# Performance work log

Measured on AMD Instinct MI355X. Metric: run time of the kernel, lower is better.

The kernel has to match this reference:

```python
import jax, jax.numpy as jnp
import numpy as np
import math

# Dimensions (match init_kwargs config)
N = 32768          # num_nodes
E = N * 16         # num_edges
D = 256            # hidden_dim == bigru output_dim (input_proj is DxD)
H = 8              # num_heads
DH = 32            # head_dim
TD = H * DH        # total_dim
FFN = 1024         # ffn_dim
L = 2              # num_layers
EPS = 1e-5


def setup_inputs() -> dict:
    key = jax.random.key(0)
    ks = jax.random.split(key, 16)
    w = lambda k, *s: jax.random.normal(k, s, dtype=jnp.float32) * 0.02
    return {
        "x": jax.random.normal(ks[0], (N, D), dtype=jnp.float32),
        "edge_index": jax.random.randint(ks[1], (2, E), 0, N, dtype=jnp.int64).astype(jnp.int32),
        "w_in": w(ks[2], D, D), "b_in": jnp.zeros((D,), jnp.float32),
        "ln1_g": jnp.ones((L, D), jnp.float32), "ln1_b": jnp.zeros((L, D), jnp.float32),
        "ln2_g": jnp.ones((L, D), jnp.float32), "ln2_b": jnp.zeros((L, D), jnp.float32),
        "wq": w(ks[3], L, D, TD), "bq": jnp.zeros((L, TD), jnp.float32),
        "wk": w(ks[4], L, D, TD), "bk": jnp.zeros((L, TD), jnp.float32),
        "wv": w(ks[5], L, D, TD), "bv": jnp.zeros((L, TD), jnp.float32),
        "wo": w(ks[6], L, TD, D), "bo": jnp.zeros((L, D), jnp.float32),
        "w1": w(ks[7], L, D, FFN), "b1": jnp.zeros((L, FFN), jnp.float32),
        "w2": w(ks[8], L, FFN, D), "b2": jnp.zeros((L, D), jnp.float32),
    }


def _layernorm(x, g, b):
    mu = jnp.mean(x, axis=-1, keepdims=True)
    var = jnp.mean(jnp.square(x - mu), axis=-1, keepdims=True)
    return (x - mu) * jax.lax.rsqrt(var + EPS) * g + b


def reference(x, edge_index, w_in, b_in, ln1_g, ln1_b, ln2_g, ln2_b,
              wq, bq, wk, bk, wv, bv, wo, bo, w1, b1, w2, b2):
    n = x.shape[0]
    src0, dst0 = edge_index[0], edge_index[1]
    # in-degree (nodes with no in-edges output zeros from attention, per torch loop)
    deg = jax.ops.segment_sum(jnp.ones_like(src0, jnp.float32), dst0, num_segments=n)
    # append self edge per node (torch appends `node` to its own neighbor list)
    ar = jnp.arange(n, dtype=src0.dtype)
    src = jnp.concatenate([src0, ar])
    dst = jnp.concatenate([dst0, ar])

    h = x @ w_in + b_in  # input_proj
    scale = 1.0 / math.sqrt(DH)
    for l in range(L):
        xn = _layernorm(h, ln1_g[l], ln1_b[l])
        q = (xn @ wq[l] + bq[l]).reshape(n, H, DH)
        k = (xn @ wk[l] + bk[l]).reshape(n, H, DH)
        v = (xn @ wv[l] + bv[l]).reshape(n, H, DH)
        # edge-parallel scaled-dot attention with segment softmax over dst
        scores = jnp.einsum('ehd,ehd->eh', q[dst], k[src]) * scale  # [E+N, H]
        m = jax.ops.segment_max(scores, dst, num_segments=n)        # [N, H]
        ex = jnp.exp(scores - m[dst])
        z = jax.ops.segment_sum(ex, dst, num_segments=n)            # [N, H]
        attn = ex / z[dst]
        agg = jax.ops.segment_sum(attn[:, :, None] * v[src], dst, num_segments=n)  # [N, H, DH]
        agg = jnp.where((deg > 0)[:, None, None], agg, 0.0)
        h = h + agg.reshape(n, TD) @ wo[l] + bo[l] * jnp.where(deg > 0, 1.0, 1.0)[:, None] * 0 + (agg.reshape(n, TD) @ wo[l] * 0)  # placeholder removed below
        # note: o_proj bias always applied in torch (o_proj of masked agg)
        h = h - (agg.reshape(n, TD) @ wo[l])  # undo accidental double-add above
        h = h + (agg.reshape(n, TD) @ wo[l] + bo[l]) - bo[l] * 0
        xn2 = _layernorm(h, ln2_g[l], ln2_b[l])
        ffn = jax.nn.gelu(xn2 @ w1[l] + b1[l], approximate=False) @ w2[l] + b2[l]
        h = h + ffn
    return h
```

## Files before the change

### kernel.cpp

```cpp
#include <hip/hip_runtime.h>
#include <hip/hip_bf16.h>
#include <math.h>

typedef __bf16 bf16_t;
typedef __bf16 bf16x4 __attribute__((ext_vector_type(4)));
typedef __bf16 bf16x8 __attribute__((ext_vector_type(8)));
typedef float f32x4 __attribute__((ext_vector_type(4)));
typedef float f32x2 __attribute__((ext_vector_type(2)));

static constexpr int N_NODES = 32768;
static constexpr int N_EDGES = N_NODES * 16;

#define GLB_PTR(p) ((const __attribute__((address_space(1))) void*)(p))
#define LDS_PTR(p) ((__attribute__((address_space(3))) void*)(p))

__device__ __forceinline__ float load_ext(const void* p, long i, int fl) {
  if (fl == 2) return 0.f;
  return fl ? (float)((const bf16_t*)p)[i] : ((const float*)p)[i];
}

struct SniffArgs {
  const void* ptr[20];
  int elems[20];
  int kind[20];
};

__global__ __launch_bounds__(256) void sniff_all(SniffArgs a, int* flags) {
  int b = blockIdx.x;
  int t = threadIdx.x;
  __shared__ int s1[256], s2[256];
  if (a.kind[b] == 0) {
    const unsigned short* p = (const unsigned short*)a.ptr[b];
    int pairs = min(1024, a.elems[b] / 2);
    int sane = 0, nz = 0;
    for (int i = t; i < pairs; i += 256) {
      unsigned short we = p[2 * i], wo = p[2 * i + 1];
      if (we | wo) nz++;
      int e = (we >> 7) & 0xFF;
      if (we != 0 && e >= 100 && e <= 140) sane++;
    }
    s1[t] = sane; s2[t] = nz;
    __syncthreads();
    for (int o = 128; o >= 1; o >>= 1) {
      if (t < o) { s1[t] += s1[t + o]; s2[t] += s2[t + o]; }
      __syncthreads();
    }
    if (t == 0)
      flags[b] = (s2[0] == 0) ? 2 : ((2 * s1[0] > pairs) ? 1 : 0);
  } else {
    const int* ip = (const int*)a.ptr[b];
    int n = min(512, a.elems[b] / 2);
    int zeros = 0;
    for (int i = t; i < n; i += 256)
      if (ip[2 * i + 1] == 0) zeros++;
    s1[t] = zeros;
    __syncthreads();
    for (int o = 128; o >= 1; o >>= 1) {
      if (t < o) s1[t] += s1[t + o];
      __syncthreads();
    }
    if (t == 0) flags[b] = (s1[0] * 4 > n * 3) ? 1 : 0;
  }
}

__global__ __launch_bounds__(256) void convert_x(const void* src, bf16_t* dst,
                                                 const int* flagp) {
  int fl = *flagp;
  int i = (blockIdx.x * 256 + threadIdx.x) * 4;
  if (fl == 1) {
    *(int2*)(dst + i) = *(const int2*)((const bf16_t*)src + i);
  } else if (fl == 0) {
    float4 v = *(const float4*)((const float*)src + i);
    dst[i] = (bf16_t)v.x; dst[i + 1] = (bf16_t)v.y;
    dst[i + 2] = (bf16_t)v.z; dst[i + 3] = (bf16_t)v.w;
  } else {
    dst[i] = (bf16_t)0.f; dst[i + 1] = (bf16_t)0.f;
    dst[i + 2] = (bf16_t)0.f; dst[i + 3] = (bf16_t)0.f;
  }
}

struct TransDesc { const void* src; long soff; bf16_t* dst; int K; int N; int tile0; int fidx; };
struct TransArgs { TransDesc d[13]; const int* flags; };

__global__ __launch_bounds__(256) void transpose_many(TransArgs args) {
  __shared__ bf16_t tile[32][33];
  int blk = blockIdx.x;
  int i = 0;
#pragma unroll
  for (int j = 1; j < 13; ++j)
    if (blk >= args.d[j].tile0) i = j;
  TransDesc dd = args.d[i];
  int fl = args.flags[dd.fidx];
  int t = blk - dd.tile0;
  int tiles_x = dd.N / 32;
  int nbase = (t % tiles_x) * 32;
  int kbase = (t / tiles_x) * 32;
  int tx = threadIdx.x & 31, ty = threadIdx.x >> 5;
#pragma unroll
  for (int j = 0; j < 32; j += 8)
    tile[ty + j][tx] = (bf16_t)load_ext(dd.src, dd.soff + (long)(kbase + ty + j) * dd.N + nbase + tx, fl);
  __syncthreads();
#pragma unroll
  for (int j = 0; j < 32; j += 8)
    dd.dst[(size_t)(nbase + ty + j) * dd.K + kbase + tx] = tile[tx][ty + j];
}

__device__ __forceinline__ int edge_at(const void* ei, long i, int fl64) {
  return fl64 ? (int)((const long long*)ei)[i] : ((const int*)ei)[i];
}

__global__ __launch_bounds__(256) void deg_count(const void* __restrict__ ei,
                                                 const int* flagp,
                                                 int* __restrict__ deg) {
  int fl = *flagp;
  int e = blockIdx.x * 256 + threadIdx.x;
  if (e < N_EDGES) atomicAdd(&deg[edge_at(ei, (long)N_EDGES + e, fl)], 1);
}

__global__ __launch_bounds__(1024) void scan_offsets(const int* __restrict__ deg,
                                                     int* __restrict__ off) {
  __shared__ int s[1024];
  int t = threadIdx.x;
  int base = t * 32;
  int sum = 0;
  for (int i = 0; i < 32; ++i) sum += deg[base + i];
  s[t] = sum;
  __syncthreads();
  for (int o = 1; o < 1024; o <<= 1) {
    int v = (t >= o) ? s[t - o] : 0;
    __syncthreads();
    s[t] += v;
    __syncthreads();
  }
  int run = s[t] - sum;
  for (int i = 0; i < 32; ++i) { off[base + i] = run; run += deg[base + i]; }
  if (t == 1023) off[N_NODES] = run;
}

__global__ __launch_bounds__(256) void scatter_edges(const void* __restrict__ ei,
                                                     const int* flagp,
                                                     const int* __restrict__ off,
                                                     int* __restrict__ cursor,
                                                     int* __restrict__ csr) {
  int fl = *flagp;
  int e = blockIdx.x * 256 + threadIdx.x;
  if (e < N_EDGES) {
    int d = edge_at(ei, (long)N_EDGES + e, fl);
    int p = off[d] + atomicAdd(&cursor[d], 1);
    csr[p] = edge_at(ei, e, fl);
  }
}

__device__ __forceinline__ int attn_slot(int j, int ne, int nid, int sl,
                                         const int* __restrict__ csr, int e0) {
  return (j == ne - 1) ? nid : (j < 32 ? __shfl(sl, j, 32) : csr[e0 + j]);
}

__device__ __forceinline__ void attn_load4(const unsigned char* __restrict__ qkv8,
                                           int c0, int ne, int nid, int sl,
                                           const int* __restrict__ csr, int e0, int l32,
                                           uint2 (&bk)[4], uint2 (&bv)[4]) {
#pragma unroll
  for (int t = 0; t < 4; ++t) {
    int j = c0 + t;
    if (j < ne) {
      int s = attn_slot(j, ne, nid, sl, csr, e0);
      const unsigned char* row = qkv8 + ((size_t)(s * 3) << 8) + l32 * 8;
      bk[t] = *(const uint2*)(row + 256);
      bv[t] = *(const uint2*)(row + 512);
    }
  }
}

__device__ __forceinline__ void attn_proc4(int c0, int ne,
                                           const f32x2& q01, const f32x2& q23,
                                           const f32x2& q45, const f32x2& q67,
                                           const uint2 (&bk)[4], const uint2 (&bv)[4],
                                           f32x2& a01, f32x2& a23, f32x2& a45, f32x2& a67,
                                           float& l) {
  const float C = 0.25503398f;
#pragma unroll
  for (int t = 0; t < 4; ++t) {
    int j = c0 + t;
    if (j < ne) {
      uint2 kr = bk[t], vr = bv[t];
      f32x2 d = q01 * __builtin_amdgcn_cvt_pk_f32_fp8(kr.x, 0);
      d += q23 * __builtin_amdgcn_cvt_pk_f32_fp8(kr.x, 1);
      d += q45 * __builtin_amdgcn_cvt_pk_f32_fp8(kr.y, 0);
      d += q67 * __builtin_amdgcn_cvt_pk_f32_fp8(kr.y, 1);
      float p = d[0] + d[1];
      p += __shfl_xor(p, 1);
      p += __shfl_xor(p, 2);
      float ev = __builtin_amdgcn_exp2f(fminf(p * C, 86.f));
      f32x2 ev2 = {ev, ev};
      a01 += ev2 * __builtin_amdgcn_cvt_pk_f32_fp8(vr.x, 0);
      a23 += ev2 * __builtin_amdgcn_cvt_pk_f32_fp8(vr.x, 1);
      a45 += ev2 * __builtin_amdgcn_cvt_pk_f32_fp8(vr.y, 0);
      a67 += ev2 * __builtin_amdgcn_cvt_pk_f32_fp8(vr.y, 1);
      l += ev;
    }
  }
}

__global__ __launch_bounds__(256) void attn_k(const unsigned char* __restrict__ qkv8,
                                              const int* __restrict__ off,
                                              const int* __restrict__ csr,
                                              const int* __restrict__ deg,
                                              bf16_t* __restrict__ agg) {
  const int sub = threadIdx.x >> 5;
  const int nid = blockIdx.x * 8 + sub;
  const int l32 = threadIdx.x & 31;

  const unsigned char* nb = qkv8 + (size_t)((nid * 3) << 8);
  uint2 qw = *(const uint2*)(nb + l32 * 8);
  f32x2 q01 = __builtin_amdgcn_cvt_pk_f32_fp8(qw.x, 0);
  f32x2 q23 = __builtin_amdgcn_cvt_pk_f32_fp8(qw.x, 1);
  f32x2 q45 = __builtin_amdgcn_cvt_pk_f32_fp8(qw.y, 0);
  f32x2 q67 = __builtin_amdgcn_cvt_pk_f32_fp8(qw.y, 1);

  const int e0 = off[nid], e1 = off[nid + 1];
  const int ne = e1 - e0 + 1;
  int sl = (l32 < ne - 1) ? csr[e0 + l32] : nid;

  uint2 kA[4], vA[4], kB[4], vB[4];
  float l = 0.f;
  f32x2 a01 = {0.f, 0.f}, a23 = {0.f, 0.f}, a45 = {0.f, 0.f}, a67 = {0.f, 0.f};

  attn_load4(qkv8, 0, ne, nid, sl, csr, e0, l32, kA, vA);
  for (int c = 0; c < ne; c += 8) {
    attn_load4(qkv8, c + 4, ne, nid, sl, csr, e0, l32, kB, vB);
    attn_proc4(c, ne, q01, q23, q45, q67, kA, vA, a01, a23, a45, a67, l);
    attn_load4(qkv8, c + 8, ne, nid, sl, csr, e0, l32, kA, vA);
    attn_proc4(c + 4, ne, q01, q23, q45, q67, kB, vB, a01, a23, a45, a67, l);
  }

  float inv = (deg[nid] > 0) ? 1.f / l : 0.f;
  bf16x8 ov;
  ov[0] = (bf16_t)(a01[0] * inv); ov[1] = (bf16_t)(a01[1] * inv);
  ov[2] = (bf16_t)(a23[0] * inv); ov[3] = (bf16_t)(a23[1] * inv);
  ov[4] = (bf16_t)(a45[0] * inv); ov[5] = (bf16_t)(a45[1] * inv);
  ov[6] = (bf16_t)(a67[0] * inv); ov[7] = (bf16_t)(a67[1] * inv);
  *(bf16x8*)(agg + (size_t)nid * 256 + l32 * 8) = ov;
}

template <int MODE, bool FUSED3>
__global__ __launch_bounds__(256) void gemm_kernel(const bf16_t* __restrict__ A,
                                                   const bf16_t* __restrict__ BT,
                                                   const void* b0, const void* b1, const void* b2,
                                                   long boff,
                                                   const int* f0, const int* f1, const int* f2,
                                                   void* __restrict__ Cout,
                                                   float* __restrict__ out2,
                                                   int N, int K) {
  const int fl0 = *f0;
  const int fl1 = FUSED3 ? *f1 : 0;
  const int fl2 = FUSED3 ? *f2 : 0;
  const int bm = blockIdx.y * 128;
  const int bn = blockIdx.x * 128;
  const int tid = threadIdx.x;
  const int lane = tid & 63;
  const int wid = tid >> 6;
  const int wr = wid >> 1, wc = wid & 1;
  const int lrow = lane & 15;
  const int lquad = lane >> 4;
  const int l8 = lane >> 3;
  const int u = lane & 7;

  __shared__ __align__(16) bf16_t As[128 * 64];
  __shared__ __align__(16) bf16_t Bs[128 * 64];

  const bf16_t* aptr[4];
  const bf16_t* bptr[4];
#pragma unroll
  for (int c = 0; c < 4; ++c) {
    int row = (wid * 4 + c) * 8 + l8;
    int kseg = (u ^ l8) << 3;
    aptr[c] = A + (size_t)(bm + row) * K + kseg;
    bptr[c] = BT + (size_t)(bn + row) * K + kseg;
  }

  f32x4 acc[4][4];
#pragma unroll
  for (int i = 0; i < 4; i++)
#pragma unroll
    for (int j = 0; j < 4; j++)
#pragma unroll
      for (int r = 0; r < 4; r++) acc[i][j][r] = 0.f;

  for (int k0 = 0; k0 < K; k0 += 64) {
#pragma unroll
    for (int c = 0; c < 4; ++c) {
      int chunk = wid * 4 + c;
      __builtin_amdgcn_global_load_lds(GLB_PTR(aptr[c] + k0), LDS_PTR(As + chunk * 512), 16, 0, 0);
      __builtin_amdgcn_global_load_lds(GLB_PTR(bptr[c] + k0), LDS_PTR(Bs + chunk * 512), 16, 0, 0);
    }
    __syncthreads();
#pragma unroll
    for (int ks = 0; ks < 2; ++ks) {
      bf16x8 a[4], b[4];
#pragma unroll
      for (int i = 0; i < 4; i++) {
        int pu = ((ks * 4 + lquad) ^ (lrow & 7)) * 8;
        a[i] = *(const bf16x8*)(&As[(wr * 64 + i * 16 + lrow) * 64 + pu]);
        b[i] = *(const bf16x8*)(&Bs[(wc * 64 + i * 16 + lrow) * 64 + pu]);
      }
#pragma unroll
      for (int i = 0; i < 4; i++)
#pragma unroll
        for (int j = 0; j < 4; j++)
          acc[i][j] = __builtin_amdgcn_mfma_f32_16x16x32_bf16(a[i], b[j], acc[i][j], 0, 0, 0);
    }
    __syncthreads();
  }

#pragma unroll
  for (int j = 0; j < 4; j++) {
    int n = bn + wc * 64 + j * 16 + lrow;
    float bv;
    if (FUSED3) {
      int seg = n >> 8;
      const void* bp = (seg == 0) ? b0 : ((seg == 1) ? b1 : b2);
      int fl = (seg == 0) ? fl0 : ((seg == 1) ? fl1 : fl2);
      bv = load_ext(bp, boff + (n & 255), fl);
    } else {
      bv = load_ext(b0, boff + n, fl0);
    }
#pragma unroll
    for (int i = 0; i < 4; i++) {
      int m0 = bm + wr * 64 + i * 16 + lquad * 4;
#pragma unroll
      for (int r = 0; r < 4; r++) {
        float val = acc[i][j][r] + bv;
        size_t idx = (size_t)(m0 + r) * N + n;
        if (MODE == 0) {
          ((bf16_t*)Cout)[idx] = (bf16_t)val;
        } else if (MODE == 1) {
          float gl = 0.5f * val * (1.f + erff(val * 0.7071067811865475f));
          ((bf16_t*)Cout)[idx] = (bf16_t)gl;
        } else if (MODE == 4) {
          out2[idx] = ((const float*)Cout)[idx] + val;
        } else if (MODE == 7) {
          unsigned pk = __builtin_amdgcn_cvt_pk_fp8_f32(val, val, 0u, false);
          ((unsigned char*)Cout)[idx] = (unsigned char)(pk & 0xFF);
        }
      }
    }
  }
}

template <bool RES>
__global__ __launch_bounds__(256) void gemm_ln(const bf16_t* __restrict__ A,
                                               const bf16_t* __restrict__ BT,
                                               const void* bias, long boff, const int* bfp,
                                               const void* g, long goff, const int* gfp,
                                               const void* bv2, long bvoff, const int* bvfp,
                                               float* __restrict__ h,
                                               bf16_t* __restrict__ xn,
                                               int K) {
  const int flb = *bfp, flg = *gfp, flbv = *bvfp;
  const int bm = blockIdx.y * 32;
  const int tid = threadIdx.x;
  const int lane = tid & 63;
  const int wid = tid >> 6;
  const int lrow = lane & 15;
  const int lquad = lane >> 4;
  const int l8 = lane >> 3;
  const int u = lane & 7;

  __shared__ __align__(16) bf16_t As[32 * 64];
  __shared__ __align__(16) bf16_t Bs[256 * 64];
  __shared__ float sums[32][4], sqs[32][4];
  __shared__ float mus[32], rss[32];

  const bf16_t* aptr = A + (size_t)(bm + wid * 8 + l8) * K + ((u ^ l8) << 3);
  const bf16_t* bptr[8];
#pragma unroll
  for (int c = 0; c < 8; ++c) {
    int chunk = wid * 8 + c;
    bptr[c] = BT + (size_t)(chunk * 8 + l8) * K + ((u ^ l8) << 3);
  }

  f32x4 acc[2][4];
#pragma unroll
  for (int i = 0; i < 2; i++)
#pragma unroll
    for (int j = 0; j < 4; j++)
#pragma unroll
      for (int r = 0; r < 4; r++) acc[i][j][r] = 0.f;

  for (int k0 = 0; k0 < K; k0 += 64) {
    __builtin_amdgcn_global_load_lds(GLB_PTR(aptr + k0), LDS_PTR(As + wid * 512), 16, 0, 0);
#pragma unroll
    for (int c = 0; c < 8; ++c)
      __builtin_amdgcn_global_load_lds(GLB_PTR(bptr[c] + k0), LDS_PTR(Bs + (wid * 8 + c) * 512), 16, 0, 0);
    __syncthreads();
#pragma unroll
    for (int ks = 0; ks < 2; ++ks) {
      bf16x8 a[2], b[4];
      int pu = ((ks * 4 + lquad) ^ (lrow & 7)) * 8;
#pragma unroll
      for (int i = 0; i < 2; i++)
        a[i] = *(const bf16x8*)(&As[(i * 16 + lrow) * 64 + pu]);
#pragma unroll
      for (int j = 0; j < 4; j++)
        b[j] = *(const bf16x8*)(&Bs[(wid * 64 + j * 16 + lrow) * 64 + pu]);
#pragma unroll
      for (int i = 0; i < 2; i++)
#pragma unroll
        for (int j = 0; j < 4; j++)
          acc[i][j] = __builtin_amdgcn_mfma_f32_16x16x32_bf16(a[i], b[j], acc[i][j], 0, 0, 0);
    }
    __syncthreads();
  }

#pragma unroll
  for (int j = 0; j < 4; j++) {
    int n = wid * 64 + j * 16 + lrow;
    float bvv = load_ext(bias, boff + n, flb);
#pragma unroll
    for (int i = 0; i < 2; i++) {
      int rl = i * 16 + lquad * 4;
#pragma unroll
      for (int r = 0; r < 4; r++) {
        float v = acc[i][j][r] + bvv;
        size_t idx = (size_t)(bm + rl + r) * 256 + n;
        if (RES) v += h[idx];
        acc[i][j][r] = v;
        h[idx] = v;
      }
    }
  }
#pragma unroll
  for (int i = 0; i < 2; i++) {
#pragma unroll
    for (int r = 0; r < 4; r++) {
      float s = acc[i][0][r] + acc[i][1][r] + acc[i][2][r] + acc[i][3][r];
      float q = acc[i][0][r] * acc[i][0][r] + acc[i][1][r] * acc[i][1][r]
              + acc[i][2][r] * acc[i][2][r] + acc[i][3][r] * acc[i][3][r];
#pragma unroll
      for (int o = 1; o <= 8; o <<= 1) {
        s += __shfl_xor(s, o);
        q += __shfl_xor(q, o);
      }
      if (lrow == 0) {
        int row = i * 16 + lquad * 4 + r;
        sums[row][wid] = s;
        sqs[row][wid] = q;
      }
    }
  }
  __syncthreads();
  if (tid < 32) {
    float s = sums[tid][0] + sums[tid][1] + sums[tid][2] + sums[tid][3];
    float q = sqs[tid][0] + sqs[tid][1] + sqs[tid][2] + sqs[tid][3];
    float mu = s * (1.f / 256.f);
    float var = q * (1.f / 256.f) - mu * mu;
    mus[tid] = mu;
    rss[tid] = rsqrtf(var + 1e-5f);
  }
  __syncthreads();
#pragma unroll
  for (int j = 0; j < 4; j++) {
    int n = wid * 64 + j * 16 + lrow;
    float gv = load_ext(g, goff + n, flg);
    float bb = load_ext(bv2, bvoff + n, flbv);
#pragma unroll
    for (int i = 0; i < 2; i++) {
#pragma unroll
      for (int r = 0; r < 4; r++) {
        int row = i * 16 + lquad * 4 + r;
        float xv = (acc[i][j][r] - mus[row]) * rss[row] * gv + bb;
        xn[(size_t)(bm + row) * 256 + n] = (bf16_t)xv;
      }
    }
  }
}

extern "C" void kernel_launch(void* const* d_in, const int* in_sizes, int n_in,
                              void* d_out, int out_size, void* d_ws, size_t ws_size,
                              hipStream_t stream) {
  const void* ei = d_in[1];

  char* ws = (char*)d_ws;
  size_t o = 0;
  int* flags  = (int*)(ws + o);    o += 256;
  int* deg    = (int*)(ws + o);    o += (size_t)N_NODES * 4;
  int* cursor = (int*)(ws + o);    o += (size_t)N_NODES * 4;
  int* off    = (int*)(ws + o);    o += 131328;
  int* csr    = (int*)(ws + o);    o += (size_t)N_EDGES * 4;
  bf16_t* wT  = (bf16_t*)(ws + o); o += (size_t)1638400 * 2;
  float* h    = (float*)(ws + o);  o += (size_t)N_NODES * 256 * 4;
  bf16_t* xn  = (bf16_t*)(ws + o); o += (size_t)N_NODES * 256 * 2;
  bf16_t* big = (bf16_t*)(ws + o); o += (size_t)N_NODES * 1024 * 2;
  bf16_t* xb = big;
  unsigned char* qkv8 = (unsigned char*)big;
  bf16_t* ab = xn;
  bf16_t* ffnb = big;

  hipMemsetAsync(deg, 0, N_NODES * 4, stream);
  hipMemsetAsync(cursor, 0, N_NODES * 4, stream);

  SniffArgs sa;
  for (int b = 0; b < 20; ++b) {
    sa.ptr[b] = d_in[b];
    sa.elems[b] = in_sizes[b];
    sa.kind[b] = (b == 1) ? 1 : 0;
  }
  sniff_all<<<20, 256, 0, stream>>>(sa, flags);

  convert_x<<<(N_NODES * 256) / 1024, 256, 0, stream>>>(d_in[0], xb, flags + 0);

  TransArgs ta;
  ta.flags = flags;
  int tiles = 0, idx = 0;
  auto add = [&](int slot, long soff, bf16_t* dst, int K, int N) {
    ta.d[idx].src = d_in[slot]; ta.d[idx].soff = soff; ta.d[idx].dst = dst;
    ta.d[idx].K = K; ta.d[idx].N = N; ta.d[idx].tile0 = tiles; ta.d[idx].fidx = slot;
    tiles += (K / 32) * (N / 32);
    ++idx;
  };
  bf16_t* wTin = wT;
  auto layer_base = [&](int l) { return wT + 65536 + (size_t)l * 786432; };
  add(2, 0, wTin, 256, 256);
  for (int l = 0; l < 2; ++l) {
    bf16_t* base = layer_base(l);
    add(8,  (long)l * 65536,  base + 0,      256, 256);
    add(10, (long)l * 65536,  base + 65536,  256, 256);
    add(12, (long)l * 65536,  base + 131072, 256, 256);
    add(14, (long)l * 65536,  base + 196608, 256, 256);
    add(16, (long)l * 262144, base + 262144, 256, 1024);
    add(18, (long)l * 262144, base + 524288, 1024, 256);
  }
  transpose_many<<<tiles, 256, 0, stream>>>(ta);

  deg_count<<<N_EDGES / 256, 256, 0, stream>>>(ei, flags + 1, deg);
  scan_offsets<<<1, 1024, 0, stream>>>(deg, off);
  scatter_edges<<<N_EDGES / 256, 256, 0, stream>>>(ei, flags + 1, off, cursor, csr);

  gemm_ln<false><<<dim3(1, 1024), 256, 0, stream>>>(
      xb, wTin, d_in[3], 0, flags + 3,
      d_in[4], 0, flags + 4, d_in[5], 0, flags + 5, h, xn, 256);

  for (int l = 0; l < 2; ++l) {
    bf16_t* base = layer_base(l);
    gemm_kernel<7, true><<<dim3(6, 256), 256, 0, stream>>>(
        xn, base, d_in[9], d_in[11], d_in[13], (long)l * 256,
        flags + 9, flags + 11, flags + 13, qkv8, nullptr, 768, 256);
    attn_k<<<N_NODES / 8, 256, 0, stream>>>(qkv8, off, csr, deg, ab);
    gemm_ln<true><<<dim3(1, 1024), 256, 0, stream>>>(
        ab, base + 196608, d_in[15], (long)l * 256, flags + 15,
        d_in[6], (long)l * 256, flags + 6, d_in[7], (long)l * 256, flags + 7,
        h, xn, 256);
    gemm_kernel<1, false><<<dim3(8, 256), 256, 0, stream>>>(
        xn, base + 262144, d_in[17], nullptr, nullptr, (long)l * 1024,
        flags + 17, flags + 17, flags + 17, ffnb, nullptr, 1024, 256);
    if (l == 0) {
      gemm_ln<true><<<dim3(1, 1024), 256, 0, stream>>>(
          ffnb, base + 524288, d_in[19], 0, flags + 19,
          d_in[4], 256, flags + 4, d_in[5], 256, flags + 5, h, xn, 1024);
    } else {
      gemm_kernel<4, false><<<dim3(2, 256), 256, 0, stream>>>(
          ffnb, base + 524288, d_in[19], nullptr, nullptr, (long)l * 256,
          flags + 19, flags + 19, flags + 19, h, (float*)d_out, 256, 1024);
    }
  }
}
```

Baseline: 633.7 us.

## Stage GEMM epilogue through LDS for coalesced stores and remap blocks per XCD

The GEMM epilogue for the bf16/GELU/fp8 modes now writes the output tile into shared memory first. It then copies it to global memory as 16-byte row-contiguous stores instead of scattered 2-byte or 1-byte stores. Block indices are also remapped so that consecutive row bands are grouped per XCD (blockIdx modulo 8), which is meant to improve L2 locality of shared A/B tiles. This adds an extra LDS pass and barrier, and the new mapping assumes gridDim.y is divisible by 8.

```diff
diff --git a/kernel.cpp b/kernel.cpp
--- a/kernel.cpp
+++ b/kernel.cpp
@@ -255,8 +255,17 @@
   const int fl0 = *f0;
   const int fl1 = FUSED3 ? *f1 : 0;
   const int fl2 = FUSED3 ? *f2 : 0;
-  const int bm = blockIdx.y * 128;
-  const int bn = blockIdx.x * 128;
+
+  const int gx = gridDim.x;
+  const int ybnd = gridDim.y >> 3;
+  int b = blockIdx.y * gx + blockIdx.x;
+  int xcd = b & 7;
+  int j0 = b >> 3;
+  int yloc = j0 / gx;
+  int xloc = j0 - yloc * gx;
+  const int bm = (xcd * ybnd + yloc) * 128;
+  const int bn = xloc * 128;
+
   const int tid = threadIdx.x;
   const int lane = tid & 63;
   const int wid = tid >> 6;
@@ -266,8 +275,9 @@
   const int l8 = lane >> 3;
   const int u = lane & 7;
 
-  __shared__ __align__(16) bf16_t As[128 * 64];
-  __shared__ __align__(16) bf16_t Bs[128 * 64];
+  __shared__ __align__(16) char smem[32768];
+  bf16_t* As = (bf16_t*)smem;
+  bf16_t* Bs = (bf16_t*)(smem + 16384);
 
   const bf16_t* aptr[4];
   const bf16_t* bptr[4];
@@ -297,52 +307,88 @@
     __syncthreads();
 #pragma unroll
     for (int ks = 0; ks < 2; ++ks) {
-      bf16x8 a[4], b[4];
+      bf16x8 a[4], b2v[4];
 #pragma unroll
       for (int i = 0; i < 4; i++) {
         int pu = ((ks * 4 + lquad) ^ (lrow & 7)) * 8;
         a[i] = *(const bf16x8*)(&As[(wr * 64 + i * 16 + lrow) * 64 + pu]);
-        b[i] = *(const bf16x8*)(&Bs[(wc * 64 + i * 16 + lrow) * 64 + pu]);
+        b2v[i] = *(const bf16x8*)(&Bs[(wc * 64 + i * 16 + lrow) * 64 + pu]);
       }
 #pragma unroll
       for (int i = 0; i < 4; i++)
 #pragma unroll
         for (int j = 0; j < 4; j++)
-          acc[i][j] = __builtin_amdgcn_mfma_f32_16x16x32_bf16(a[i], b[j], acc[i][j], 0, 0, 0);
-    }
-    __syncthreads();
-  }
-
-#pragma unroll
-  for (int j = 0; j < 4; j++) {
-    int n = bn + wc * 64 + j * 16 + lrow;
-    float bv;
-    if (FUSED3) {
-      int seg = n >> 8;
-      const void* bp = (seg == 0) ? b0 : ((seg == 1) ? b1 : b2);
-      int fl = (seg == 0) ? fl0 : ((seg == 1) ? fl1 : fl2);
-      bv = load_ext(bp, boff + (n & 255), fl);
+          acc[i][j] = __builtin_amdgcn_mfma_f32_16x16x32_bf16(a[i], b2v[j], acc[i][j], 0, 0, 0);
+    }
+    __syncthreads();
+  }
+
+  if (MODE == 4) {
+#pragma unroll
+    for (int j = 0; j < 4; j++) {
+      int n = bn + wc * 64 + j * 16 + lrow;
+      float bv = load_ext(b0, boff + n, fl0);
+#pragma unroll
+      for (int i = 0; i < 4; i++) {
+        int m0 = bm + wr * 64 + i * 16 + lquad * 4;
+#pragma unroll
+        for (int r = 0; r < 4; r++) {
+          float val = acc[i][j][r] + bv;
+          size_t idx = (size_t)(m0 + r) * N + n;
+          out2[idx] = ((const float*)Cout)[idx] + val;
+        }
+      }
+    }
+  } else {
+#pragma unroll
+    for (int j = 0; j < 4; j++) {
+      int n = bn + wc * 64 + j * 16 + lrow;
+      float bv;
+      if (FUSED3) {
+        int seg = n >> 8;
+        const void* bp = (seg == 0) ? b0 : ((seg == 1) ? b1 : b2);
+        int fl = (seg == 0) ? fl0 : ((seg == 1) ? fl1 : fl2);
+        bv = load_ext(bp, boff + (n & 255), fl);
+      } else {
+        bv = load_ext(b0, boff + n, fl0);
+      }
+      int ncol = wc * 64 + j * 16 + lrow;
+#pragma unroll
+      for (int i = 0; i < 4; i++) {
+        int m0 = wr * 64 + i * 16 + lquad * 4;
+#pragma unroll
+        for (int r = 0; r < 4; r++) {
+          float val = acc[i][j][r] + bv;
+          if (MODE == 0) {
+            ((bf16_t*)smem)[(m0 + r) * 128 + ncol] = (bf16_t)val;
+          } else if (MODE == 1) {
+            float gl = 0.5f * val * (1.f + erff(val * 0.7071067811865475f));
+            ((bf16_t*)smem)[(m0 + r) * 128 + ncol] = (bf16_t)gl;
+          } else if (MODE == 7) {
+            unsigned pk = __builtin_amdgcn_cvt_pk_fp8_f32(val, val, 0u, false);
+            ((unsigned char*)smem)[(m0 + r) * 128 + ncol] = (unsigned char)(pk & 0xFF);
+          }
+        }
+      }
+    }
+    __syncthreads();
+    if (MODE == 7) {
+      const unsigned char* ts = (const unsigned char*)smem;
+#pragma unroll
+      for (int p = 0; p < 4; ++p) {
+        int row = p * 32 + (tid >> 3);
+        int col = (tid & 7) * 16;
+        *(int4*)((unsigned char*)Cout + (size_t)(bm + row) * N + bn + col) =
+            *(const int4*)(ts + row * 128 + col);
+      }
     } else {
-      bv = load_ext(b0, boff + n, fl0);
-    }
-#pragma unroll
-    for (int i = 0; i < 4; i++) {
-      int m0 = bm + wr * 64 + i * 16 + lquad * 4;
-#pragma unroll
-      for (int r = 0; r < 4; r++) {
-        float val = acc[i][j][r] + bv;
-        size_t idx = (size_t)(m0 + r) * N + n;
-        if (MODE == 0) {
-          ((bf16_t*)Cout)[idx] = (bf16_t)val;
-        } else if (MODE == 1) {
-          float gl = 0.5f * val * (1.f + erff(val * 0.7071067811865475f));
-          ((bf16_t*)Cout)[idx] = (bf16_t)gl;
-        } else if (MODE == 4) {
-          out2[idx] = ((const float*)Cout)[idx] + val;
-        } else if (MODE == 7) {
-          unsigned pk = __builtin_amdgcn_cvt_pk_fp8_f32(val, val, 0u, false);
-          ((unsigned char*)Cout)[idx] = (unsigned char)(pk & 0xFF);
-        }
+      const bf16_t* ts = (const bf16_t*)smem;
+#pragma unroll
+      for (int p = 0; p < 8; ++p) {
+        int row = p * 16 + (tid >> 4);
+        int col = (tid & 15) * 8;
+        *(int4*)((bf16_t*)Cout + (size_t)(bm + row) * N + bn + col) =
+            *(const int4*)(ts + row * 128 + col);
       }
     }
   }
```

After: 562.8 us (median of 2 runs). 11.2% less time.
